# Kernel optimization log

Hardware: AMD Instinct MI355X
Metric: run time of the kernel (lower is better)

## Reference

```python
import jax, jax.numpy as jnp
import numpy as np

D = 2048   # dec_hidden_size == enc_hidden_size
IN = 512   # input_size
T = 4096   # T_enc


def setup_inputs() -> dict:
    key = jax.random.key(0)
    ks = jax.random.split(key, 20)
    s = 0.02
    zeros = jnp.zeros
    return {
        "data": jax.random.normal(ks[0], (1, IN), jnp.float32),
        "h0": jax.random.normal(ks[1], (1, 1, D), jnp.float32),
        "c0": jax.random.normal(ks[2], (1, 1, D), jnp.float32),
        "enc_output": jax.random.normal(ks[3], (T, 1, D), jnp.float32),
        "pi": jax.random.normal(ks[4], (T,), jnp.float32),
        "W_w": jax.random.normal(ks[5], (D, D), jnp.float32) * s,
        "U_w": jax.random.normal(ks[6], (D, D), jnp.float32) * s,
        "V_w": jax.random.normal(ks[7], (1, D), jnp.float32) * s,
        "lin_w": jax.random.normal(ks[8], (D, D), jnp.float32) * s,
        "lin_b": zeros((D,), jnp.float32),
        "lin1_w": jax.random.normal(ks[9], (D, D), jnp.float32) * s,
        "lin1_b": zeros((D,), jnp.float32),
        "lin2_w": jax.random.normal(ks[10], (D, D), jnp.float32) * s,
        "lin2_b": zeros((D,), jnp.float32),
        "dense_w": jax.random.normal(ks[11], (1, D), jnp.float32) * s,
        "dense_b": zeros((1,), jnp.float32),
        "W_ih": jax.random.normal(ks[12], (4 * D, IN + D), jnp.float32) * s,
        "W_hh": jax.random.normal(ks[13], (4 * D, D), jnp.float32) * s,
        "b_ih": zeros((4 * D,), jnp.float32),
        "b_hh": zeros((4 * D,), jnp.float32),
        "i": 100,
    }


def reference(data, h0, c0, enc_output, pi, W_w, U_w, V_w, lin_w, lin_b,
              lin1_w, lin1_b, lin2_w, lin2_b, dense_w, dense_b,
              W_ih, W_hh, b_ih, b_hh, i):
    Tl = pi.shape[0]
    output_pos = i + 1
    enc = enc_output[:, 0, :]                      # (T, E)
    # binary_vector(output_pos, T) @ pi : row k gets pi[output_pos+T-k-2] iff k >= output_pos-1
    k = jnp.arange(Tl)
    idx = output_pos + Tl - k - 2
    prod = jnp.where(k >= output_pos - 1, pi[jnp.clip(idx, 0, Tl - 1)], 0.0)
    u_h = (enc @ U_w.T) * prod[:, None]            # (T, D), per-channel scale by prod
    q = h0[0, 0] @ W_w.T                           # (D,)
    score = jnp.tanh(q[None, :] + u_h) @ V_w[0]    # (T,)
    score = jnp.where(k < output_pos, 0.0, score)  # attn_score[:j_null] = 0 (zero, not -inf)
    attn = jax.nn.softmax(score)                   # softmax over T
    context = attn @ enc                           # (E,)
    x = jnp.concatenate([context, data[0]])        # (E + IN,)
    # single-step LSTM, PyTorch gate order i,f,g,o
    gates = x @ W_ih.T + b_ih + h0[0, 0] @ W_hh.T + b_hh
    gi, gf, gg, go = jnp.split(gates, 4)
    c_new = jax.nn.sigmoid(gf) * c0[0, 0] + jax.nn.sigmoid(gi) * jnp.tanh(gg)
    h_new = jax.nn.sigmoid(go) * jnp.tanh(c_new)
    fc = h_new @ lin_w.T + lin_b
    l1 = fc @ lin1_w.T + lin1_b
    delta = jax.nn.softmax(l1)
    beta = jax.nn.softplus(fc @ lin2_w.T + lin2_b)
    gamma = l1 @ dense_w.T + dense_b               # original reuses linear1 for lin3
    return (gamma, beta, delta, h_new, c_new)
```

## Files before the change

### kernel.cpp

```cpp
#include <hip/hip_runtime.h>
#include <hip/hip_bf16.h>

#define D_  2048
#define IN_ 512
#define T_  4096
#define G4_ 8192

typedef __attribute__((ext_vector_type(4))) float f32x4;
typedef __attribute__((ext_vector_type(8))) short s16x8;

#define WS_PROD    0
#define WS_Q       (T_)
#define WS_X       (T_ + D_)
#define WS_PARTIAL (WS_X + D_ + IN_)
#define WS_SCORE   (WS_PARTIAL + T_*16)
#define WS_ATTN    (WS_SCORE + T_)
#define WS_GATES   (WS_ATTN + T_)
#define WS_G2      (WS_GATES + G4_)
#define WS_FC      (WS_G2 + G4_)
#define WS_L1      (WS_FC + D_)
#define WS_HN      (WS_L1 + D_)

__device__ inline short bfbits(__hip_bfloat16 h) {
  union { __hip_bfloat16 b; short s; } u; u.b = h; return u.s;
}

__device__ inline float wave_dot4(const float* __restrict__ w,
                                  const float* __restrict__ x, int n4, int lane) {
  float s = 0.f;
  const f32x4* w4 = (const f32x4*)w;
  const f32x4* x4 = (const f32x4*)x;
  for (int c = lane; c < n4; c += 64) {
    f32x4 a = w4[c], b = x4[c];
    s += a[0]*b[0] + a[1]*b[1] + a[2]*b[2] + a[3]*b[3];
  }
  #pragma unroll
  for (int m = 32; m >= 1; m >>= 1) s += __shfl_xor(s, m, 64);
  return s;
}

__global__ __launch_bounds__(256) void k_prep(const float* __restrict__ Ww,
    const float* __restrict__ h0, const float* __restrict__ pi,
    const float* __restrict__ data, const int* __restrict__ ip,
    float* __restrict__ ws) {
  const int tid = threadIdx.x, bid = blockIdx.x;
  const int gidx = bid * 256 + tid;
  const int op = ip[0] + 1;
  if (gidx < T_) {
    float p = 0.f;
    if (gidx >= op - 1) {
      int idx = op + T_ - gidx - 2;
      idx = idx < 0 ? 0 : (idx > T_ - 1 ? T_ - 1 : idx);
      p = pi[idx];
    }
    ws[WS_PROD + gidx] = p;
  }
  if (gidx < IN_) ws[WS_X + D_ + gidx] = data[gidx];
  const int wid = tid >> 6, lane = tid & 63;
  const int row = bid * 4 + wid;
  if (row < D_) {
    float s = wave_dot4(Ww + (size_t)row * D_, h0, D_ / 4, lane);
    if (lane == 0) ws[WS_Q + row] = s;
  }
}

__global__ __launch_bounds__(512, 4) void k_gemm_score(
    const float* __restrict__ enc, const float* __restrict__ Uw,
    const float* __restrict__ Vw, const float* __restrict__ h0,
    const float* __restrict__ Whh, float* __restrict__ ws) {
  __shared__ __align__(16) short sbuf[2 * 128 * 40];
  short* Ah = sbuf;
  short* Bh = sbuf + 128 * 40;
  const int tid = threadIdx.x;
  const int lane = tid & 63, wid = tid >> 6;
  const int wr = wid >> 2, wc = wid & 3;
  const int g = lane >> 4, lr = lane & 15;
  const int mb = blockIdx.x, nb = blockIdx.y;

  f32x4 acc[4][2];
  #pragma unroll
  for (int m = 0; m < 4; ++m)
    #pragma unroll
    for (int n = 0; n < 2; ++n) acc[m][n] = (f32x4){0.f, 0.f, 0.f, 0.f};

  const int srow = tid >> 2;
  const int scol = (tid & 3) * 8;
  const float* pa0 = enc + (size_t)(mb * 128 + srow) * D_ + scol;
  const float* pb0 = Uw  + (size_t)(nb * 128 + srow) * D_ + scol;
  const int sidx = srow * 40 + scol;

  f32x4 an0 = *(const f32x4*)(pa0);
  f32x4 an1 = *(const f32x4*)(pa0 + 4);
  f32x4 bn0 = *(const f32x4*)(pb0);
  f32x4 bn1 = *(const f32x4*)(pb0 + 4);

  for (int ks = 0; ks < 64; ++ks) {
    f32x4 a0 = an0, a1 = an1, b0 = bn0, b1 = bn1;
    if (ks < 63) {
      an0 = *(const f32x4*)(pa0 + (ks + 1) * 32);
      an1 = *(const f32x4*)(pa0 + (ks + 1) * 32 + 4);
      bn0 = *(const f32x4*)(pb0 + (ks + 1) * 32);
      bn1 = *(const f32x4*)(pb0 + (ks + 1) * 32 + 4);
    }
    __syncthreads();
    __align__(16) short ah[8], bh[8];
    #pragma unroll
    for (int e = 0; e < 4; ++e) {
      ah[e]     = bfbits(__float2bfloat16(a0[e]));
      ah[4 + e] = bfbits(__float2bfloat16(a1[e]));
      bh[e]     = bfbits(__float2bfloat16(b0[e]));
      bh[4 + e] = bfbits(__float2bfloat16(b1[e]));
    }
    *(s16x8*)&Ah[sidx] = *(s16x8*)&ah[0];
    *(s16x8*)&Bh[sidx] = *(s16x8*)&bh[0];
    __syncthreads();

    s16x8 af[4], bf[2];
    #pragma unroll
    for (int m = 0; m < 4; ++m)
      af[m] = *(const s16x8*)&Ah[(wr * 64 + m * 16 + lr) * 40 + g * 8];
    #pragma unroll
    for (int n = 0; n < 2; ++n)
      bf[n] = *(const s16x8*)&Bh[(wc * 32 + n * 16 + lr) * 40 + g * 8];
    #pragma unroll
    for (int m = 0; m < 4; ++m)
      #pragma unroll
      for (int n = 0; n < 2; ++n)
        acc[m][n] = __builtin_amdgcn_mfma_f32_16x16x32_bf16(af[m], bf[n], acc[m][n], 0, 0, 0);
  }

  const float* q    = ws + WS_Q;
  const float* prod = ws + WS_PROD;
  float Vv[2], qv[2];
  #pragma unroll
  for (int n = 0; n < 2; ++n) {
    const int d = nb * 128 + wc * 32 + n * 16 + lr;
    Vv[n] = Vw[d]; qv[n] = q[d];
  }
  __syncthreads();
  float* red = (float*)sbuf;
  #pragma unroll
  for (int m = 0; m < 4; ++m) {
    #pragma unroll
    for (int r = 0; r < 4; ++r) {
      const int t_loc = wr * 64 + m * 16 + g * 4 + r;
      const float p = prod[mb * 128 + t_loc];
      float s = Vv[0] * tanhf(qv[0] + p * acc[m][0][r])
              + Vv[1] * tanhf(qv[1] + p * acc[m][1][r]);
      s += __shfl_xor(s, 1, 64);
      s += __shfl_xor(s, 2, 64);
      s += __shfl_xor(s, 4, 64);
      s += __shfl_xor(s, 8, 64);
      if (lr == 0) red[t_loc * 4 + wc] = s;
    }
  }
  __syncthreads();
  if (tid < 128) {
    const float s = red[tid * 4] + red[tid * 4 + 1] + red[tid * 4 + 2] + red[tid * 4 + 3];
    ws[WS_PARTIAL + (size_t)(mb * 128 + tid) * 16 + nb] = s;
  }

  const int flat = blockIdx.y * gridDim.x + blockIdx.x;
  const int rbase = flat * 16 + wid * 2;
  #pragma unroll
  for (int rr = 0; rr < 2; ++rr) {
    const int row = rbase + rr;
    float s = wave_dot4(Whh + (size_t)row * D_, h0, D_ / 4, lane);
    if (lane == 0) ws[WS_G2 + row] = s;
  }
}

__global__ __launch_bounds__(256) void k_score(const int* __restrict__ ip,
                                               float* __restrict__ ws) {
  const int t = blockIdx.x * 256 + threadIdx.x;
  const int op = ip[0] + 1;
  const float* p = ws + WS_PARTIAL + (size_t)t * 16;
  float s = 0.f;
  #pragma unroll
  for (int c = 0; c < 16; ++c) s += p[c];
  ws[WS_SCORE + t] = (t < op) ? 0.f : s;
}

__global__ __launch_bounds__(1024) void k_attn(float* __restrict__ ws) {
  __shared__ float sm[16];
  const int tid = threadIdx.x, lane = tid & 63, wid = tid >> 6;
  float v[4];
  #pragma unroll
  for (int j = 0; j < 4; ++j) v[j] = ws[WS_SCORE + tid + j * 1024];
  float mx = fmaxf(fmaxf(v[0], v[1]), fmaxf(v[2], v[3]));
  #pragma unroll
  for (int m = 32; m >= 1; m >>= 1) mx = fmaxf(mx, __shfl_xor(mx, m, 64));
  if (lane == 0) sm[wid] = mx;
  __syncthreads();
  if (tid == 0) {
    float m2 = sm[0];
    for (int w = 1; w < 16; ++w) m2 = fmaxf(m2, sm[w]);
    sm[0] = m2;
  }
  __syncthreads();
  mx = sm[0];
  __syncthreads();
  float e[4], ls = 0.f;
  #pragma unroll
  for (int j = 0; j < 4; ++j) { e[j] = expf(v[j] - mx); ls += e[j]; }
  #pragma unroll
  for (int m = 32; m >= 1; m >>= 1) ls += __shfl_xor(ls, m, 64);
  if (lane == 0) sm[wid] = ls;
  __syncthreads();
  if (tid == 0) {
    float s2 = 0.f;
    for (int w = 0; w < 16; ++w) s2 += sm[w];
    sm[0] = s2;
  }
  __syncthreads();
  const float inv = 1.f / sm[0];
  #pragma unroll
  for (int j = 0; j < 4; ++j) ws[WS_ATTN + tid + j * 1024] = e[j] * inv;
}

__global__ __launch_bounds__(256) void k_context(const float* __restrict__ enc,
                                                 float* __restrict__ ws) {
  const int d = blockIdx.x * 256 + threadIdx.x;
  const int t0 = blockIdx.y * 256;
  const float* attn = ws + WS_ATTN;
  float s = 0.f;
  for (int t = t0; t < t0 + 256; ++t) s += attn[t] * enc[(size_t)t * D_ + d];
  atomicAdd(&ws[WS_X + d], s);
}

__global__ __launch_bounds__(256) void k_gates(const float* __restrict__ Wih,
    const float* __restrict__ bih, const float* __restrict__ bhh,
    float* __restrict__ ws) {
  const int wid = threadIdx.x >> 6, lane = threadIdx.x & 63;
  const int row = blockIdx.x * 4 + wid;
  float s = wave_dot4(Wih + (size_t)row * (D_ + IN_), ws + WS_X, (D_ + IN_) / 4, lane);
  if (lane == 0) ws[WS_GATES + row] = s + ws[WS_G2 + row] + bih[row] + bhh[row];
}

__global__ __launch_bounds__(256) void k_cell(const float* __restrict__ c0,
    float* __restrict__ ws, float* __restrict__ out) {
  const int d = blockIdx.x * 256 + threadIdx.x;
  const float* gt = ws + WS_GATES;
  const float gi = gt[d], gf = gt[D_ + d], gg = gt[2 * D_ + d], go = gt[3 * D_ + d];
  const float si = 1.f / (1.f + expf(-gi));
  const float sf = 1.f / (1.f + expf(-gf));
  const float so = 1.f / (1.f + expf(-go));
  const float cn = sf * c0[d] + si * tanhf(gg);
  const float hn = so * tanhf(cn);
  out[1 + 2 * D_ + d] = hn;
  out[1 + 3 * D_ + d] = cn;
  ws[WS_HN + d] = hn;
}

__global__ __launch_bounds__(256) void k_fc(const float* __restrict__ lw,
    const float* __restrict__ lb, float* __restrict__ ws) {
  const int wid = threadIdx.x >> 6, lane = threadIdx.x & 63;
  const int row = blockIdx.x * 4 + wid;
  float s = wave_dot4(lw + (size_t)row * D_, ws + WS_HN, D_ / 4, lane);
  if (lane == 0) ws[WS_FC + row] = s + lb[row];
}

__global__ __launch_bounds__(256) void k_l1beta(const float* __restrict__ l1w,
    const float* __restrict__ l1b, const float* __restrict__ l2w,
    const float* __restrict__ l2b, float* __restrict__ ws, float* __restrict__ out) {
  const int wid = threadIdx.x >> 6, lane = threadIdx.x & 63;
  const int row = blockIdx.x * 4 + wid;
  float a = wave_dot4(l1w + (size_t)row * D_, ws + WS_FC, D_ / 4, lane);
  float b = wave_dot4(l2w + (size_t)row * D_, ws + WS_FC, D_ / 4, lane);
  if (lane == 0) {
    ws[WS_L1 + row] = a + l1b[row];
    const float x = b + l2b[row];
    out[1 + row] = (x > 20.f) ? x : log1pf(expf(x));
  }
}

__global__ __launch_bounds__(256) void k_final(const float* __restrict__ dw,
    const float* __restrict__ db, float* __restrict__ ws, float* __restrict__ out) {
  __shared__ float sm[4];
  const int tid = threadIdx.x, lane = tid & 63, wid = tid >> 6;
  float v[8];
  #pragma unroll
  for (int j = 0; j < 8; ++j) v[j] = ws[WS_L1 + tid + j * 256];
  float mx = v[0];
  #pragma unroll
  for (int j = 1; j < 8; ++j) mx = fmaxf(mx, v[j]);
  #pragma unroll
  for (int m = 32; m >= 1; m >>= 1) mx = fmaxf(mx, __shfl_xor(mx, m, 64));
  if (lane == 0) sm[wid] = mx;
  __syncthreads();
  mx = fmaxf(fmaxf(sm[0], sm[1]), fmaxf(sm[2], sm[3]));
  __syncthreads();
  float e[8], ls = 0.f;
  #pragma unroll
  for (int j = 0; j < 8; ++j) { e[j] = expf(v[j] - mx); ls += e[j]; }
  #pragma unroll
  for (int m = 32; m >= 1; m >>= 1) ls += __shfl_xor(ls, m, 64);
  if (lane == 0) sm[wid] = ls;
  __syncthreads();
  ls = sm[0] + sm[1] + sm[2] + sm[3];
  __syncthreads();
  const float inv = 1.f / ls;
  float gp = 0.f;
  #pragma unroll
  for (int j = 0; j < 8; ++j) {
    out[1 + D_ + tid + j * 256] = e[j] * inv;
    gp += v[j] * dw[tid + j * 256];
  }
  #pragma unroll
  for (int m = 32; m >= 1; m >>= 1) gp += __shfl_xor(gp, m, 64);
  if (lane == 0) sm[wid] = gp;
  __syncthreads();
  if (tid == 0) out[0] = sm[0] + sm[1] + sm[2] + sm[3] + db[0];
}

extern "C" void kernel_launch(void* const* d_in, const int* in_sizes, int n_in,
                              void* d_out, int out_size, void* d_ws, size_t ws_size,
                              hipStream_t stream) {
  (void)in_sizes; (void)n_in; (void)out_size; (void)ws_size;
  const float* data   = (const float*)d_in[0];
  const float* h0     = (const float*)d_in[1];
  const float* c0     = (const float*)d_in[2];
  const float* enc    = (const float*)d_in[3];
  const float* pi     = (const float*)d_in[4];
  const float* Ww     = (const float*)d_in[5];
  const float* Uw     = (const float*)d_in[6];
  const float* Vw     = (const float*)d_in[7];
  const float* lin_w  = (const float*)d_in[8];
  const float* lin_b  = (const float*)d_in[9];
  const float* lin1_w = (const float*)d_in[10];
  const float* lin1_b = (const float*)d_in[11];
  const float* lin2_w = (const float*)d_in[12];
  const float* lin2_b = (const float*)d_in[13];
  const float* dw     = (const float*)d_in[14];
  const float* db     = (const float*)d_in[15];
  const float* Wih    = (const float*)d_in[16];
  const float* Whh    = (const float*)d_in[17];
  const float* bih    = (const float*)d_in[18];
  const float* bhh    = (const float*)d_in[19];
  const int*   ip     = (const int*)d_in[20];
  float* ws  = (float*)d_ws;
  float* out = (float*)d_out;

  hipMemsetAsync(ws + WS_X, 0, D_ * sizeof(float), stream);
  k_prep<<<512, 256, 0, stream>>>(Ww, h0, pi, data, ip, ws);
  k_gemm_score<<<dim3(T_ / 128, D_ / 128), 512, 0, stream>>>(enc, Uw, Vw, h0, Whh, ws);
  k_score<<<T_ / 256, 256, 0, stream>>>(ip, ws);
  k_attn<<<1, 1024, 0, stream>>>(ws);
  k_context<<<dim3(D_ / 256, T_ / 256), 256, 0, stream>>>(enc, ws);
  k_gates<<<G4_ / 4, 256, 0, stream>>>(Wih, bih, bhh, ws);
  k_cell<<<D_ / 256, 256, 0, stream>>>(c0, ws, out);
  k_fc<<<D_ / 4, 256, 0, stream>>>(lin_w, lin_b, ws);
  k_l1beta<<<D_ / 4, 256, 0, stream>>>(lin1_w, lin1_b, lin2_w, lin2_b, ws, out);
  k_final<<<1, 256, 0, stream>>>(dw, db, ws, out);
}
```

Before: 136.9 us.

## Pre-convert enc and U_w to bf16 in workspace and use direct-to-LDS GEMM loads

A prep kernel converts enc_output and U_w to bf16 in the workspace once per call. The GEMM then streams bf16 tiles with global_load_lds into XOR-swizzled LDS over a 64-wide K step, uses a remapped block order, and the context reduction reads bf16 enc. The score kernel is folded into the softmax kernel and the memset is folded into prep. The aim is to halve GEMM read traffic and drop the per-tile conversion, at the cost of an extra full read and write of enc and U_w plus lower-precision context.

Measured after the change: 137.0 us. Within noise of the previous version (+0.1%).

```diff
diff --git a/kernel.cpp b/kernel.cpp
--- a/kernel.cpp
+++ b/kernel.cpp
@@ -8,21 +8,29 @@
 
 typedef __attribute__((ext_vector_type(4))) float f32x4;
 typedef __attribute__((ext_vector_type(8))) short s16x8;
+typedef unsigned short u16;
 
 #define WS_PROD    0
 #define WS_Q       (T_)
 #define WS_X       (T_ + D_)
 #define WS_PARTIAL (WS_X + D_ + IN_)
-#define WS_SCORE   (WS_PARTIAL + T_*16)
-#define WS_ATTN    (WS_SCORE + T_)
+#define WS_ATTN    (WS_PARTIAL + T_*16)
 #define WS_GATES   (WS_ATTN + T_)
 #define WS_G2      (WS_GATES + G4_)
 #define WS_FC      (WS_G2 + G4_)
 #define WS_L1      (WS_FC + D_)
 #define WS_HN      (WS_L1 + D_)
-
-__device__ inline short bfbits(__hip_bfloat16 h) {
-  union { __hip_bfloat16 b; short s; } u; u.b = h; return u.s;
+#define WS_BF16    (WS_HN + D_)
+#define WS_FAST_BYTES ((size_t)WS_BF16 * 4 + ((size_t)T_ * D_ + (size_t)D_ * D_) * 2)
+
+typedef const __attribute__((address_space(1))) void gas_t;
+typedef __attribute__((address_space(3))) void las_t;
+
+__device__ inline u16 bfbits(float f) {
+  union { __hip_bfloat16 b; u16 s; } u; u.b = __float2bfloat16(f); return u.s;
+}
+__device__ inline float bf2f(u16 s) {
+  union { unsigned u; float f; } v; v.u = ((unsigned)s) << 16; return v.f;
 }
 
 __device__ inline float wave_dot4(const float* __restrict__ w,
@@ -42,7 +50,8 @@
 __global__ __launch_bounds__(256) void k_prep(const float* __restrict__ Ww,
     const float* __restrict__ h0, const float* __restrict__ pi,
     const float* __restrict__ data, const int* __restrict__ ip,
-    float* __restrict__ ws) {
+    const float* __restrict__ enc, const float* __restrict__ Uw,
+    int do_convert, float* __restrict__ ws) {
   const int tid = threadIdx.x, bid = blockIdx.x;
   const int gidx = bid * 256 + tid;
   const int op = ip[0] + 1;
@@ -55,6 +64,7 @@
     }
     ws[WS_PROD + gidx] = p;
   }
+  if (gidx < D_) ws[WS_X + gidx] = 0.f;
   if (gidx < IN_) ws[WS_X + D_ + gidx] = data[gidx];
   const int wid = tid >> 6, lane = tid & 63;
   const int row = bid * 4 + wid;
@@ -62,20 +72,42 @@
     float s = wave_dot4(Ww + (size_t)row * D_, h0, D_ / 4, lane);
     if (lane == 0) ws[WS_Q + row] = s;
   }
-}
-
-__global__ __launch_bounds__(512, 4) void k_gemm_score(
-    const float* __restrict__ enc, const float* __restrict__ Uw,
+  if (do_convert) {
+    u16* encB = (u16*)(ws + WS_BF16);
+    u16* UwB  = encB + (size_t)T_ * D_;
+    const size_t nth = 512u * 256u;
+    for (size_t base = (size_t)gidx * 8; base < (size_t)T_ * D_; base += nth * 8) {
+      f32x4 v0 = *(const f32x4*)(enc + base);
+      f32x4 v1 = *(const f32x4*)(enc + base + 4);
+      u16 t[8];
+      #pragma unroll
+      for (int e = 0; e < 4; ++e) { t[e] = bfbits(v0[e]); t[4 + e] = bfbits(v1[e]); }
+      *(s16x8*)&encB[base] = *(s16x8*)&t[0];
+    }
+    for (size_t base = (size_t)gidx * 8; base < (size_t)D_ * D_; base += nth * 8) {
+      f32x4 v0 = *(const f32x4*)(Uw + base);
+      f32x4 v1 = *(const f32x4*)(Uw + base + 4);
+      u16 t[8];
+      #pragma unroll
+      for (int e = 0; e < 4; ++e) { t[e] = bfbits(v0[e]); t[4 + e] = bfbits(v1[e]); }
+      *(s16x8*)&UwB[base] = *(s16x8*)&t[0];
+    }
+  }
+}
+
+__global__ __launch_bounds__(512, 4) void k_gemm_bf16(
     const float* __restrict__ Vw, const float* __restrict__ h0,
     const float* __restrict__ Whh, float* __restrict__ ws) {
-  __shared__ __align__(16) short sbuf[2 * 128 * 40];
-  short* Ah = sbuf;
-  short* Bh = sbuf + 128 * 40;
-  const int tid = threadIdx.x;
-  const int lane = tid & 63, wid = tid >> 6;
+  __shared__ __align__(16) u16 Ah[128 * 64];
+  __shared__ __align__(16) u16 Bh[128 * 64];
+  const u16* encB = (const u16*)(ws + WS_BF16);
+  const u16* UwB  = encB + (size_t)T_ * D_;
+  const int tid = threadIdx.x, lane = tid & 63, wid = tid >> 6;
   const int wr = wid >> 2, wc = wid & 3;
   const int g = lane >> 4, lr = lane & 15;
-  const int mb = blockIdx.x, nb = blockIdx.y;
+  const int bid = blockIdx.x;
+  const int wgid = (bid & 7) * 64 + (bid >> 3);
+  const int mb = wgid >> 4, nb = wgid & 15;
 
   f32x4 acc[4][2];
   #pragma unroll
@@ -83,50 +115,42 @@
     #pragma unroll
     for (int n = 0; n < 2; ++n) acc[m][n] = (f32x4){0.f, 0.f, 0.f, 0.f};
 
-  const int srow = tid >> 2;
-  const int scol = (tid & 3) * 8;
-  const float* pa0 = enc + (size_t)(mb * 128 + srow) * D_ + scol;
-  const float* pb0 = Uw  + (size_t)(nb * 128 + srow) * D_ + scol;
-  const int sidx = srow * 40 + scol;
-
-  f32x4 an0 = *(const f32x4*)(pa0);
-  f32x4 an1 = *(const f32x4*)(pa0 + 4);
-  f32x4 bn0 = *(const f32x4*)(pb0);
-  f32x4 bn1 = *(const f32x4*)(pb0 + 4);
-
-  for (int ks = 0; ks < 64; ++ks) {
-    f32x4 a0 = an0, a1 = an1, b0 = bn0, b1 = bn1;
-    if (ks < 63) {
-      an0 = *(const f32x4*)(pa0 + (ks + 1) * 32);
-      an1 = *(const f32x4*)(pa0 + (ks + 1) * 32 + 4);
-      bn0 = *(const f32x4*)(pb0 + (ks + 1) * 32);
-      bn1 = *(const f32x4*)(pb0 + (ks + 1) * 32 + 4);
-    }
+  const int c0 = tid,        r0 = c0 >> 3, s0 = (c0 & 7) ^ (r0 & 7);
+  const int c1 = tid + 512,  r1 = c1 >> 3, s1 = (c1 & 7) ^ (r1 & 7);
+  const u16* ga0 = encB + (size_t)(mb * 128 + r0) * D_ + s0 * 8;
+  const u16* ga1 = encB + (size_t)(mb * 128 + r1) * D_ + s1 * 8;
+  const u16* gb0 = UwB  + (size_t)(nb * 128 + r0) * D_ + s0 * 8;
+  const u16* gb1 = UwB  + (size_t)(nb * 128 + r1) * D_ + s1 * 8;
+  u16* la0 = &Ah[c0 * 8]; u16* la1 = &Ah[c1 * 8];
+  u16* lb0 = &Bh[c0 * 8]; u16* lb1 = &Bh[c1 * 8];
+
+  for (int ks = 0; ks < D_ / 64; ++ks) {
     __syncthreads();
-    __align__(16) short ah[8], bh[8];
-    #pragma unroll
-    for (int e = 0; e < 4; ++e) {
-      ah[e]     = bfbits(__float2bfloat16(a0[e]));
-      ah[4 + e] = bfbits(__float2bfloat16(a1[e]));
-      bh[e]     = bfbits(__float2bfloat16(b0[e]));
-      bh[4 + e] = bfbits(__float2bfloat16(b1[e]));
-    }
-    *(s16x8*)&Ah[sidx] = *(s16x8*)&ah[0];
-    *(s16x8*)&Bh[sidx] = *(s16x8*)&bh[0];
+    __builtin_amdgcn_global_load_lds((gas_t*)(ga0 + ks * 64), (las_t*)la0, 16, 0, 0);
+    __builtin_amdgcn_global_load_lds((gas_t*)(ga1 + ks * 64), (las_t*)la1, 16, 0, 0);
+    __builtin_amdgcn_global_load_lds((gas_t*)(gb0 + ks * 64), (las_t*)lb0, 16, 0, 0);
+    __builtin_amdgcn_global_load_lds((gas_t*)(gb1 + ks * 64), (las_t*)lb1, 16, 0, 0);
     __syncthreads();
-
-    s16x8 af[4], bf[2];
-    #pragma unroll
-    for (int m = 0; m < 4; ++m)
-      af[m] = *(const s16x8*)&Ah[(wr * 64 + m * 16 + lr) * 40 + g * 8];
-    #pragma unroll
-    for (int n = 0; n < 2; ++n)
-      bf[n] = *(const s16x8*)&Bh[(wc * 32 + n * 16 + lr) * 40 + g * 8];
-    #pragma unroll
-    for (int m = 0; m < 4; ++m)
-      #pragma unroll
-      for (int n = 0; n < 2; ++n)
-        acc[m][n] = __builtin_amdgcn_mfma_f32_16x16x32_bf16(af[m], bf[n], acc[m][n], 0, 0, 0);
+    #pragma unroll
+    for (int kk = 0; kk < 2; ++kk) {
+      const int koff = kk * 64 + g * 16;
+      s16x8 af[4], bf[2];
+      #pragma unroll
+      for (int m = 0; m < 4; ++m) {
+        const int r = wr * 64 + m * 16 + lr;
+        af[m] = *(const s16x8*)((const char*)Ah + r * 128 + (koff ^ ((r & 7) << 4)));
+      }
+      #pragma unroll
+      for (int n = 0; n < 2; ++n) {
+        const int r = wc * 32 + n * 16 + lr;
+        bf[n] = *(const s16x8*)((const char*)Bh + r * 128 + (koff ^ ((r & 7) << 4)));
+      }
+      #pragma unroll
+      for (int m = 0; m < 4; ++m)
+        #pragma unroll
+        for (int n = 0; n < 2; ++n)
+          acc[m][n] = __builtin_amdgcn_mfma_f32_16x16x32_bf16(af[m], bf[n], acc[m][n], 0, 0, 0);
+    }
   }
 
   const float* q    = ws + WS_Q;
@@ -138,7 +162,7 @@
     Vv[n] = Vw[d]; qv[n] = q[d];
   }
   __syncthreads();
-  float* red = (float*)sbuf;
+  float* red = (float*)Ah;
   #pragma unroll
   for (int m = 0; m < 4; ++m) {
     #pragma unroll
@@ -160,8 +184,7 @@
     ws[WS_PARTIAL + (size_t)(mb * 128 + tid) * 16 + nb] = s;
   }
 
-  const int flat = blockIdx.y * gridDim.x + blockIdx.x;
-  const int rbase = flat * 16 + wid * 2;
+  const int rbase = bid * 16 + wid * 2;
   #pragma unroll
   for (int rr = 0; rr < 2; ++rr) {
     const int row = rbase + rr;
@@ -170,23 +193,124 @@
   }
 }
 
-__global__ __launch_bounds__(256) void k_score(const int* __restrict__ ip,
+__global__ __launch_bounds__(512, 4) void k_gemm_f32(
+    const float* __restrict__ enc, const float* __restrict__ Uw,
+    const float* __restrict__ Vw, const float* __restrict__ h0,
+    const float* __restrict__ Whh, float* __restrict__ ws) {
+  __shared__ __align__(16) u16 sbuf[2 * 128 * 40];
+  u16* Ah = sbuf;
+  u16* Bh = sbuf + 128 * 40;
+  const int tid = threadIdx.x;
+  const int lane = tid & 63, wid = tid >> 6;
+  const int wr = wid >> 2, wc = wid & 3;
+  const int g = lane >> 4, lr = lane & 15;
+  const int mb = blockIdx.x, nb = blockIdx.y;
+
+  f32x4 acc[4][2];
+  #pragma unroll
+  for (int m = 0; m < 4; ++m)
+    #pragma unroll
+    for (int n = 0; n < 2; ++n) acc[m][n] = (f32x4){0.f, 0.f, 0.f, 0.f};
+
+  const int srow = tid >> 2;
+  const int scol = (tid & 3) * 8;
+  const float* pa0 = enc + (size_t)(mb * 128 + srow) * D_ + scol;
+  const float* pb0 = Uw  + (size_t)(nb * 128 + srow) * D_ + scol;
+  const int sidx = srow * 40 + scol;
+
+  f32x4 an0 = *(const f32x4*)(pa0);
+  f32x4 an1 = *(const f32x4*)(pa0 + 4);
+  f32x4 bn0 = *(const f32x4*)(pb0);
+  f32x4 bn1 = *(const f32x4*)(pb0 + 4);
+
+  for (int ks = 0; ks < 64; ++ks) {
+    f32x4 a0 = an0, a1 = an1, b0 = bn0, b1 = bn1;
+    if (ks < 63) {
+      an0 = *(const f32x4*)(pa0 + (ks + 1) * 32);
+      an1 = *(const f32x4*)(pa0 + (ks + 1) * 32 + 4);
+      bn0 = *(const f32x4*)(pb0 + (ks + 1) * 32);
+      bn1 = *(const f32x4*)(pb0 + (ks + 1) * 32 + 4);
+    }
+    __syncthreads();
+    __align__(16) u16 ah[8], bh[8];
+    #pragma unroll
+    for (int e = 0; e < 4; ++e) {
+      ah[e] = bfbits(a0[e]); ah[4 + e] = bfbits(a1[e]);
+      bh[e] = bfbits(b0[e]); bh[4 + e] = bfbits(b1[e]);
+    }
+    *(s16x8*)&Ah[sidx] = *(s16x8*)&ah[0];
+    *(s16x8*)&Bh[sidx] = *(s16x8*)&bh[0];
+    __syncthreads();
+
+    s16x8 af[4], bf[2];
+    #pragma unroll
+    for (int m = 0; m < 4; ++m)
+      af[m] = *(const s16x8*)&Ah[(wr * 64 + m * 16 + lr) * 40 + g * 8];
+    #pragma unroll
+    for (int n = 0; n < 2; ++n)
+      bf[n] = *(const s16x8*)&Bh[(wc * 32 + n * 16 + lr) * 40 + g * 8];
+    #pragma unroll
+    for (int m = 0; m < 4; ++m)
+      #pragma unroll
+      for (int n = 0; n < 2; ++n)
+        acc[m][n] = __builtin_amdgcn_mfma_f32_16x16x32_bf16(af[m], bf[n], acc[m][n], 0, 0, 0);
+  }
+
+  const float* q    = ws + WS_Q;
+  const float* prod = ws + WS_PROD;
+  float Vv[2], qv[2];
+  #pragma unroll
+  for (int n = 0; n < 2; ++n) {
+    const int d = nb * 128 + wc * 32 + n * 16 + lr;
+    Vv[n] = Vw[d]; qv[n] = q[d];
+  }
+  __syncthreads();
+  float* red = (float*)sbuf;
+  #pragma unroll
+  for (int m = 0; m < 4; ++m) {
+    #pragma unroll
+    for (int r = 0; r < 4; ++r) {
+      const int t_loc = wr * 64 + m * 16 + g * 4 + r;
+      const float p = prod[mb * 128 + t_loc];
+      float s = Vv[0] * tanhf(qv[0] + p * acc[m][0][r])
+              + Vv[1] * tanhf(qv[1] + p * acc[m][1][r]);
+      s += __shfl_xor(s, 1, 64);
+      s += __shfl_xor(s, 2, 64);
+      s += __shfl_xor(s, 4, 64);
+      s += __shfl_xor(s, 8, 64);
+      if (lr == 0) red[t_loc * 4 + wc] = s;
+    }
+  }
+  __syncthreads();
+  if (tid < 128) {
+    const float s = red[tid * 4] + red[tid * 4 + 1] + red[tid * 4 + 2] + red[tid * 4 + 3];
+    ws[WS_PARTIAL + (size_t)(mb * 128 + tid) * 16 + nb] = s;
+  }
+  const int flat = blockIdx.y * gridDim.x + blockIdx.x;
+  const int rbase = flat * 16 + wid * 2;
+  #pragma unroll
+  for (int rr = 0; rr < 2; ++rr) {
+    const int row = rbase + rr;
+    float s = wave_dot4(Whh + (size_t)row * D_, h0, D_ / 4, lane);
+    if (lane == 0) ws[WS_G2 + row] = s;
+  }
+}
+
+__global__ __launch_bounds__(1024) void k_attn(const int* __restrict__ ip,
                                                float* __restrict__ ws) {
-  const int t = blockIdx.x * 256 + threadIdx.x;
-  const int op = ip[0] + 1;
-  const float* p = ws + WS_PARTIAL + (size_t)t * 16;
-  float s = 0.f;
-  #pragma unroll
-  for (int c = 0; c < 16; ++c) s += p[c];
-  ws[WS_SCORE + t] = (t < op) ? 0.f : s;
-}
-
-__global__ __launch_bounds__(1024) void k_attn(float* __restrict__ ws) {
   __shared__ float sm[16];
   const int tid = threadIdx.x, lane = tid & 63, wid = tid >> 6;
+  const int op = ip[0] + 1;
   float v[4];
   #pragma unroll
-  for (int j = 0; j < 4; ++j) v[j] = ws[WS_SCORE + tid + j * 1024];
+  for (int j = 0; j < 4; ++j) {
+    const int t = tid + j * 1024;
+    const float* p = ws + WS_PARTIAL + (size_t)t * 16;
+    float s = 0.f;
+    #pragma unroll
+    for (int c = 0; c < 16; ++c) s += p[c];
+    v[j] = (t < op) ? 0.f : s;
+  }
   float mx = fmaxf(fmaxf(v[0], v[1]), fmaxf(v[2], v[3]));
   #pragma unroll
   for (int m = 32; m >= 1; m >>= 1) mx = fmaxf(mx, __shfl_xor(mx, m, 64));
@@ -218,8 +342,17 @@
   for (int j = 0; j < 4; ++j) ws[WS_ATTN + tid + j * 1024] = e[j] * inv;
 }
 
-__global__ __launch_bounds__(256) void k_context(const float* __restrict__ enc,
-                                                 float* __restrict__ ws) {
+__global__ __launch_bounds__(256) void k_context_bf16(float* __restrict__ ws) {
+  const u16* encB = (const u16*)(ws + WS_BF16);
+  const int d = blockIdx.x * 256 + threadIdx.x;
+  const int t0 = blockIdx.y * 256;
+  const float* attn = ws + WS_ATTN;
+  float s = 0.f;
+  for (int t = t0; t < t0 + 256; ++t) s += attn[t] * bf2f(encB[(size_t)t * D_ + d]);
+  atomicAdd(&ws[WS_X + d], s);
+}
+__global__ __launch_bounds__(256) void k_context_f32(const float* __restrict__ enc,
+                                                     float* __restrict__ ws) {
   const int d = blockIdx.x * 256 + threadIdx.x;
   const int t0 = blockIdx.y * 256;
   const float* attn = ws + WS_ATTN;
@@ -316,7 +449,7 @@
 extern "C" void kernel_launch(void* const* d_in, const int* in_sizes, int n_in,
                               void* d_out, int out_size, void* d_ws, size_t ws_size,
                               hipStream_t stream) {
-  (void)in_sizes; (void)n_in; (void)out_size; (void)ws_size;
+  (void)in_sizes; (void)n_in; (void)out_size;
   const float* data   = (const float*)d_in[0];
   const float* h0     = (const float*)d_in[1];
   const float* c0     = (const float*)d_in[2];
@@ -340,13 +473,18 @@
   const int*   ip     = (const int*)d_in[20];
   float* ws  = (float*)d_ws;
   float* out = (float*)d_out;
-
-  hipMemsetAsync(ws + WS_X, 0, D_ * sizeof(float), stream);
-  k_prep<<<512, 256, 0, stream>>>(Ww, h0, pi, data, ip, ws);
-  k_gemm_score<<<dim3(T_ / 128, D_ / 128), 512, 0, stream>>>(enc, Uw, Vw, h0, Whh, ws);
-  k_score<<<T_ / 256, 256, 0, stream>>>(ip, ws);
-  k_attn<<<1, 1024, 0, stream>>>(ws);
-  k_context<<<dim3(D_ / 256, T_ / 256), 256, 0, stream>>>(enc, ws);
+  const int fast = (ws_size >= WS_FAST_BYTES) ? 1 : 0;
+
+  k_prep<<<512, 256, 0, stream>>>(Ww, h0, pi, data, ip, enc, Uw, fast, ws);
+  if (fast)
+    k_gemm_bf16<<<512, 512, 0, stream>>>(Vw, h0, Whh, ws);
+  else
+    k_gemm_f32<<<dim3(T_ / 128, D_ / 128), 512, 0, stream>>>(enc, Uw, Vw, h0, Whh, ws);
+  k_attn<<<1, 1024, 0, stream>>>(ip, ws);
+  if (fast)
+    k_context_bf16<<<dim3(D_ / 256, T_ / 256), 256, 0, stream>>>(ws);
+  else
+    k_context_f32<<<dim3(D_ / 256, T_ / 256), 256, 0, stream>>>(enc, ws);
   k_gates<<<G4_ / 4, 256, 0, stream>>>(Wih, bih, bhh, ws);
   k_cell<<<D_ / 256, 256, 0, stream>>>(c0, ws, out);
   k_fc<<<D_ / 4, 256, 0, stream>>>(lin_w, lin_b, ws);
```
